# Optimization experiments

Hardware: AMD Instinct MI355X
Metric: run time of the kernel (lower is better)

## Reference

```python
import jax, jax.numpy as jnp
import numpy as np

N_NODES = 50000
N_EDGES = 800000
DIM = 128


def setup_inputs() -> dict:
    key = jax.random.key(0)
    k_x, k_e, k_w1, k_w2 = jax.random.split(key, 4)
    x = jax.random.normal(k_x, (N_NODES, DIM), dtype=jnp.float32)
    edge_index = jax.random.randint(k_e, (2, N_EDGES), 0, N_NODES, dtype=jnp.int64)
    scale = 1.0 / np.sqrt(DIM)
    W1 = jax.random.normal(k_w1, (DIM, DIM), dtype=jnp.float32) * scale
    b1 = jnp.zeros((DIM,), dtype=jnp.float32)
    W2 = jax.random.normal(k_w2, (DIM, DIM), dtype=jnp.float32) * scale
    b2 = jnp.zeros((DIM,), dtype=jnp.float32)
    return {"x": x, "edge_index": edge_index, "W1": W1, "b1": b1, "W2": W2, "b2": b2}


def _gcn_conv(x, W, b, src, dst, n_nodes):
    """PyG GCNConv: D^{-1/2}(A+I)D^{-1/2} (x @ W) + b, self-loops added."""
    h = x @ W  # [N, D]
    ones = jnp.ones(src.shape[0], dtype=h.dtype)
    # degree of A+I, counting incoming edges at target nodes plus self-loop
    deg = jax.ops.segment_sum(ones, dst, num_segments=n_nodes) + 1.0
    dinv = jax.lax.rsqrt(deg)  # [N]
    norm = dinv[src] * dinv[dst]  # [E]
    msgs = h[src] * norm[:, None]  # [E, D] gather (memory-bound)
    agg = jax.ops.segment_sum(msgs, dst, num_segments=n_nodes)  # scatter-add
    agg = agg + h * (dinv * dinv)[:, None]  # self-loop contribution
    return agg + b


def reference(x, edge_index, W1, b1, W2, b2):
    src, dst = edge_index[0], edge_index[1]
    n = x.shape[0]
    identity = x
    out = jax.nn.relu(_gcn_conv(x, W1, b1, src, dst, n))
    out = _gcn_conv(out, W2, b2, src, dst, n)
    return jax.nn.relu(out + identity)
```

## Files before the change

kernel.cpp:

```cpp
#include <hip/hip_runtime.h>

#define N_NODES 50000
#define N_EDGES 800000
#define DIM 128
#define NB 391
#define CAP 2560
#define NCH 7
#define BIN_CHUNK 4096
#define BIN_BLOCKS 196
#define GEMM_TILES 782

typedef unsigned int uint;
typedef unsigned short ushort;
typedef __attribute__((ext_vector_type(8))) __bf16 bf16x8;
typedef __attribute__((ext_vector_type(4))) float f32x4;

__device__ __forceinline__ uint f2bf(float f) {
    uint u = __float_as_uint(f);
    return (u + 0x7FFFu + ((u >> 16) & 1u)) >> 16;
}
__device__ __forceinline__ float2 bf2f2(uint u) {
    return make_float2(__uint_as_float(u << 16), __uint_as_float(u & 0xFFFF0000u));
}


__global__ __launch_bounds__(256) void prep_kernel(const float* __restrict__ W1,
                                                   const float* __restrict__ W2,
                                                   uint* __restrict__ Wt1,
                                                   uint* __restrict__ Wt2,
                                                   int* __restrict__ bincursor) {
    int idx = blockIdx.x * 256 + threadIdx.x;
    if (idx < 16384) {
        const float* W = (idx < 8192) ? W1 : W2;
        uint* Wt = (idx < 8192) ? Wt1 : Wt2;
        int i = idx & 8191;
        int n = i >> 6, k2 = i & 63;
        Wt[i] = f2bf(W[(2 * k2) * DIM + n]) | (f2bf(W[(2 * k2 + 1) * DIM + n]) << 16);
    } else {
        int b = idx - 16384;
        if (b < NB) bincursor[b] = b * CAP;
    }
}


template <bool ABF, bool SCALE, bool FROM_LDS>
__device__ __forceinline__ void gemm_tile(const void* Xv, const uint* __restrict__ sB,
                                          const uint* __restrict__ Wt,
                                          const float* __restrict__ dinv, int base,
                                          uint* __restrict__ Hout) {
    int t = threadIdx.x;
    int wv = t >> 6;
    int l = t & 63;
    int col = l & 15;
    int g = l >> 4;
    int lr = wv * 16 + col;
    int grow = base + lr;

    bf16x8 af[4];
    if (FROM_LDS) {
#pragma unroll
        for (int kk = 0; kk < 4; ++kk) {
            int ui = lr * 64 + ((kk * 16 + g * 4) ^ ((lr & 7) << 2));
            af[kk] = __builtin_bit_cast(bf16x8, *(const uint4*)&sB[ui]);
        }
    } else {
        int ar = grow > N_NODES - 1 ? N_NODES - 1 : grow;
        if (ABF) {
            const uint4* Xr = (const uint4*)((const uint*)Xv + (size_t)ar * 64);
#pragma unroll
            for (int kk = 0; kk < 4; ++kk) af[kk] = __builtin_bit_cast(bf16x8, Xr[kk * 4 + g]);
        } else {
            const float4* Xr = (const float4*)((const float*)Xv + (size_t)ar * DIM);
#pragma unroll
            for (int kk = 0; kk < 4; ++kk) {
                float4 x0 = Xr[kk * 8 + g * 2];
                float4 x1 = Xr[kk * 8 + g * 2 + 1];
                uint4 p;
                p.x = f2bf(x0.x) | (f2bf(x0.y) << 16);
                p.y = f2bf(x0.z) | (f2bf(x0.w) << 16);
                p.z = f2bf(x1.x) | (f2bf(x1.y) << 16);
                p.w = f2bf(x1.z) | (f2bf(x1.w) << 16);
                af[kk] = __builtin_bit_cast(bf16x8, p);
            }
        }
    }

    const uint4* Wr = (const uint4*)Wt;
    f32x4 acc[8];
#pragma unroll
    for (int n = 0; n < 8; ++n) acc[n] = (f32x4){0.f, 0.f, 0.f, 0.f};

#pragma unroll
    for (int n = 0; n < 8; ++n) {
        const uint4* wrow = Wr + (size_t)(n * 16 + col) * 16;
#pragma unroll
        for (int kk = 0; kk < 4; ++kk) {
            bf16x8 bf = __builtin_bit_cast(bf16x8, wrow[kk * 4 + g]);
            acc[n] = __builtin_amdgcn_mfma_f32_16x16x32_bf16(af[kk], bf, acc[n], 0, 0, 0);
        }
    }

#pragma unroll
    for (int j = 0; j < 4; ++j) {
        int row = base + wv * 16 + g * 4 + j;
        if (row < N_NODES) {
            float di = SCALE ? dinv[row] : 1.0f;
            ushort* hrow = (ushort*)(Hout + (size_t)row * 64);
#pragma unroll
            for (int n = 0; n < 8; ++n) {
                float v = SCALE ? acc[n][j] * di : acc[n][j];
                hrow[n * 16 + col] = (ushort)f2bf(v);
            }
        }
    }
}


__global__ __launch_bounds__(256) void bin_gemm1_kernel(const int* __restrict__ ei,
                                                        int* __restrict__ bincursor,
                                                        uint* __restrict__ pairs,
                                                        const float* __restrict__ x,
                                                        const uint* __restrict__ Wt1,
                                                        uint* __restrict__ Hs) {
    if (blockIdx.x >= BIN_BLOCKS) {
        int tile = blockIdx.x - BIN_BLOCKS;
        gemm_tile<false, false, false>((const void*)x, nullptr, Wt1, nullptr, tile * 64, Hs);
        return;
    }
    __shared__ int lh[NB];
    __shared__ int lbase[NB];
    int t = threadIdx.x;
    int eb = blockIdx.x * BIN_CHUNK;

    for (int b = t; b < NB; b += 256) lh[b] = 0;
    __syncthreads();

    int s_reg[16], d_reg[16];
#pragma unroll
    for (int i = 0; i < 16; ++i) {
        int e = eb + i * 256 + t;
        if (e < N_EDGES) {
            s_reg[i] = ei[e];
            d_reg[i] = ei[N_EDGES + e];
            atomicAdd(&lh[d_reg[i] >> 7], 1);
        } else {
            d_reg[i] = -1;
        }
    }
    __syncthreads();

    for (int b = t; b < NB; b += 256) {
        int c = lh[b];
        lbase[b] = c ? atomicAdd(&bincursor[b], c) : 0;
    }
    __syncthreads();
    for (int b = t; b < NB; b += 256) lh[b] = 0;
    __syncthreads();

#pragma unroll
    for (int i = 0; i < 16; ++i) {
        int d = d_reg[i];
        if (d >= 0) {
            int bin = d >> 7;
            int r = atomicAdd(&lh[bin], 1);
            pairs[lbase[bin] + r] = ((uint)s_reg[i] << 7) | (uint)(d & 127);
        }
    }
}


__global__ __launch_bounds__(256) void fill2_kernel(const uint* __restrict__ pairs,
                                                    const int* __restrict__ bincursor,
                                                    int* __restrict__ rowbeg,
                                                    int* __restrict__ rowend,
                                                    float* __restrict__ dinv,
                                                    int* __restrict__ csr_src) {
    __shared__ int cnt[128 * 8];
    __shared__ int nsum[128];
    __shared__ int nbase[128];
    int t = threadIdx.x;
    int blk = blockIdx.x;
    int bs = blk * CAP;
    int be = bincursor[blk];

    for (int i = t; i < 128 * 8; i += 256) cnt[i] = 0;
    __syncthreads();

    for (int p = bs + t; p < be; p += 256) {
        uint pr = pairs[p];
        atomicAdd(&cnt[(pr & 127u) * 8 + (pr >> 20)], 1);
    }
    __syncthreads();

    if (t < 128) {
        int s = 0;
#pragma unroll
        for (int c = 0; c < NCH; ++c) s += cnt[t * 8 + c];
        nsum[t] = s;
        nbase[t] = s;
    }
    __syncthreads();
#pragma unroll
    for (int off = 1; off < 128; off <<= 1) {
        int v = (t < 128 && t >= off) ? nbase[t - off] : 0;
        __syncthreads();
        if (t < 128) nbase[t] += v;
        __syncthreads();
    }

    if (t < 128) {
        int ex = nbase[t] - nsum[t];
        int node = blk * 128 + t;
        if (node < N_NODES) {
            rowbeg[node] = bs + ex;
            rowend[node] = bs + nbase[t];
            dinv[node] = rsqrtf((float)nsum[t] + 1.0f);
        }
        int run = ex;
#pragma unroll
        for (int c = 0; c < NCH; ++c) {
            int v = cnt[t * 8 + c];
            cnt[t * 8 + c] = run;
            run += v;
        }
    }
    __syncthreads();

    for (int p = bs + t; p < be; p += 256) {
        uint pr = pairs[p];
        int r = atomicAdd(&cnt[(pr & 127u) * 8 + (pr >> 20)], 1);
        csr_src[bs + r] = (int)(pr >> 7);
    }
}


template <bool DSRC>
__device__ __forceinline__ void agg_node(const int* __restrict__ rowbeg,
                                         const int* __restrict__ rowend,
                                         const int* __restrict__ csr_src,
                                         const uint* __restrict__ Hs,
                                         const float* __restrict__ dinv,
                                         const float* __restrict__ bias, int node, int li,
                                         float r[8]) {
    int beg = rowbeg[node];
    int end = rowend[node];
    float di = dinv[node];

    const uint4* H4 = (const uint4*)Hs;
    float a0, a1, a2, a3, a4, a5, a6, a7;
    {
        uint4 su = H4[(size_t)node * 16 + li];
        float2 v0 = bf2f2(su.x), v1 = bf2f2(su.y), v2 = bf2f2(su.z), v3 = bf2f2(su.w);
        float sf = DSRC ? di : 1.0f;
        a0 = sf * v0.x; a1 = sf * v0.y; a2 = sf * v1.x; a3 = sf * v1.y;
        a4 = sf * v2.x; a5 = sf * v2.y; a6 = sf * v3.x; a7 = sf * v3.y;
    }

#define ADDF8(u, f)                                                               \
    {                                                                             \
        float2 v0 = bf2f2(u.x), v1 = bf2f2(u.y), v2 = bf2f2(u.z), v3 = bf2f2(u.w);\
        a0 += f * v0.x; a1 += f * v0.y; a2 += f * v1.x; a3 += f * v1.y;           \
        a4 += f * v2.x; a5 += f * v2.y; a6 += f * v3.x; a7 += f * v3.y;           \
    }

    int e = beg;
    for (; e + 3 < end; e += 4) {
        int s0 = csr_src[e], s1 = csr_src[e + 1], s2 = csr_src[e + 2], s3 = csr_src[e + 3];
        uint4 u0 = H4[(size_t)s0 * 16 + li];
        uint4 u1 = H4[(size_t)s1 * 16 + li];
        uint4 u2 = H4[(size_t)s2 * 16 + li];
        uint4 u3 = H4[(size_t)s3 * 16 + li];
        float f0 = DSRC ? dinv[s0] : 1.0f;
        float f1 = DSRC ? dinv[s1] : 1.0f;
        float f2 = DSRC ? dinv[s2] : 1.0f;
        float f3 = DSRC ? dinv[s3] : 1.0f;
        ADDF8(u0, f0);
        ADDF8(u1, f1);
        ADDF8(u2, f2);
        ADDF8(u3, f3);
    }
    for (; e < end; ++e) {
        int s = csr_src[e];
        uint4 u = H4[(size_t)s * 16 + li];
        float f = DSRC ? dinv[s] : 1.0f;
        ADDF8(u, f);
    }
#undef ADDF8

    const float4* B4 = (const float4*)bias;
    float4 bb0 = B4[li * 2], bb1 = B4[li * 2 + 1];
    r[0] = a0 * di + bb0.x; r[1] = a1 * di + bb0.y;
    r[2] = a2 * di + bb0.z; r[3] = a3 * di + bb0.w;
    r[4] = a4 * di + bb1.x; r[5] = a5 * di + bb1.y;
    r[6] = a6 * di + bb1.z; r[7] = a7 * di + bb1.w;
}


__global__ __launch_bounds__(256) void aggemm_kernel(const int* __restrict__ rowbeg,
                                                     const int* __restrict__ rowend,
                                                     const int* __restrict__ csr_src,
                                                     const uint* __restrict__ Hs,
                                                     const float* __restrict__ dinv,
                                                     const float* __restrict__ b1,
                                                     const uint* __restrict__ Wt2,
                                                     uint* __restrict__ Hs2) {
    __shared__ uint sB[64 * 64];
    int t = threadIdx.x;
    int wv = t >> 6;
    int lane = t & 63;
    int grp = lane >> 4;
    int li = lane & 15;
    int base = blockIdx.x * 64;

#pragma unroll
    for (int p = 0; p < 4; ++p) {
        int row = p * 16 + wv * 4 + grp;
        int node = base + row;
        if (node < N_NODES) {
            float r[8];
            agg_node<true>(rowbeg, rowend, csr_src, Hs, dinv, b1, node, li, r);
            uint4 o;
            o.x = f2bf(fmaxf(r[0], 0.f)) | (f2bf(fmaxf(r[1], 0.f)) << 16);
            o.y = f2bf(fmaxf(r[2], 0.f)) | (f2bf(fmaxf(r[3], 0.f)) << 16);
            o.z = f2bf(fmaxf(r[4], 0.f)) | (f2bf(fmaxf(r[5], 0.f)) << 16);
            o.w = f2bf(fmaxf(r[6], 0.f)) | (f2bf(fmaxf(r[7], 0.f)) << 16);
            int ui = row * 64 + ((li * 4) ^ ((row & 7) << 2));
            *(uint4*)&sB[ui] = o;
        }
    }
    __syncthreads();

    gemm_tile<true, true, true>(nullptr, sB, Wt2, dinv, base, Hs2);
}


__global__ __launch_bounds__(256) void agg2_kernel(const int* __restrict__ rowbeg,
                                                   const int* __restrict__ rowend,
                                                   const int* __restrict__ csr_src,
                                                   const uint* __restrict__ Hs2,
                                                   const float* __restrict__ dinv,
                                                   const float* __restrict__ b2,
                                                   const float* __restrict__ resid,
                                                   float* __restrict__ out) {
    int wave = (int)((blockIdx.x * (size_t)blockDim.x + threadIdx.x) >> 6);
    int lane = threadIdx.x & 63;
    int grp = lane >> 4;
    int li = lane & 15;
    int node = wave * 4 + grp;

    float r[8];
    agg_node<false>(rowbeg, rowend, csr_src, Hs2, dinv, b2, node, li, r);

    const float4* R4 = (const float4*)(resid + (size_t)node * DIM);
    float4 x0 = R4[li * 2], x1 = R4[li * 2 + 1];
    r[0] += x0.x; r[1] += x0.y; r[2] += x0.z; r[3] += x0.w;
    r[4] += x1.x; r[5] += x1.y; r[6] += x1.z; r[7] += x1.w;

    float4* O4 = (float4*)(out + (size_t)node * DIM);
    O4[li * 2] = make_float4(fmaxf(r[0], 0.f), fmaxf(r[1], 0.f), fmaxf(r[2], 0.f),
                             fmaxf(r[3], 0.f));
    O4[li * 2 + 1] = make_float4(fmaxf(r[4], 0.f), fmaxf(r[5], 0.f), fmaxf(r[6], 0.f),
                                 fmaxf(r[7], 0.f));
}


extern "C" void kernel_launch(void* const* d_in, const int* in_sizes, int n_in,
                              void* d_out, int out_size, void* d_ws, size_t ws_size,
                              hipStream_t stream) {
    const float* x = (const float*)d_in[0];
    const int* edge_index = (const int*)d_in[1];
    const float* W1 = (const float*)d_in[2];
    const float* b1 = (const float*)d_in[3];
    const float* W2 = (const float*)d_in[4];
    const float* b2 = (const float*)d_in[5];
    float* out = (float*)d_out;

    char* ws = (char*)d_ws;
    int*   bincursor = (int*)(ws + 0);
    float* dinv      = (float*)(ws + (64 << 10));
    int*   rowbeg    = (int*)(ws + (320 << 10));
    int*   rowend    = (int*)(ws + (576 << 10));
    int*   csr_src   = (int*)(ws + (1 << 20));
    uint*  pairs     = (uint*)(ws + (6 << 20));
    uint*  Hs        = (uint*)(ws + (11 << 20));
    uint*  Hs2       = (uint*)(ws + (24 << 20));
    uint*  Wt1       = (uint*)(ws + (37 << 20));
    uint*  Wt2       = (uint*)(ws + (37 << 20) + (64 << 10));

    prep_kernel<<<66, 256, 0, stream>>>(W1, W2, Wt1, Wt2, bincursor);
    bin_gemm1_kernel<<<BIN_BLOCKS + GEMM_TILES, 256, 0, stream>>>(edge_index, bincursor, pairs,
                                                                  x, Wt1, Hs);
    fill2_kernel<<<NB, 256, 0, stream>>>(pairs, bincursor, rowbeg, rowend, dinv, csr_src);
    aggemm_kernel<<<GEMM_TILES, 256, 0, stream>>>(rowbeg, rowend, csr_src, Hs, dinv, b1, Wt2,
                                                  Hs2);
    agg2_kernel<<<3125, 256, 0, stream>>>(rowbeg, rowend, csr_src, Hs2, dinv, b2, x, out);
}
```

Measured before the change: 124.8 us.

## Halve aggregate-GEMM tile to 32 rows and unroll edge gather by 8

The fused layer-1 aggregation plus layer-2 GEMM kernel now processes 32 nodes per block instead of 64, doubling the grid. Its GEMM is split so each of the four waves computes a 16x64 quarter of the output. The edge-gather loop in agg_node is unrolled to 8 outstanding loads, with a 4-edge tail, to raise memory-level parallelism. The trade-off is more blocks with repeated W2 reads per block, and higher register pressure from the deeper unroll.

```diff
diff --git a/kernel.cpp b/kernel.cpp
--- a/kernel.cpp
+++ b/kernel.cpp
@@ -9,6 +9,7 @@
 #define BIN_CHUNK 4096
 #define BIN_BLOCKS 196
 #define GEMM_TILES 782
+#define AGG_TILES 1563
 
 typedef unsigned int uint;
 typedef unsigned short ushort;
@@ -43,46 +44,29 @@
 }
 
 
-template <bool ABF, bool SCALE, bool FROM_LDS>
-__device__ __forceinline__ void gemm_tile(const void* Xv, const uint* __restrict__ sB,
-                                          const uint* __restrict__ Wt,
-                                          const float* __restrict__ dinv, int base,
-                                          uint* __restrict__ Hout) {
+__device__ __forceinline__ void gemm_tile64(const float* __restrict__ X,
+                                            const uint* __restrict__ Wt, int base,
+                                            uint* __restrict__ Hout) {
     int t = threadIdx.x;
     int wv = t >> 6;
     int l = t & 63;
     int col = l & 15;
     int g = l >> 4;
-    int lr = wv * 16 + col;
-    int grow = base + lr;
+    int grow = base + wv * 16 + col;
+    int ar = grow > N_NODES - 1 ? N_NODES - 1 : grow;
 
     bf16x8 af[4];
-    if (FROM_LDS) {
-#pragma unroll
-        for (int kk = 0; kk < 4; ++kk) {
-            int ui = lr * 64 + ((kk * 16 + g * 4) ^ ((lr & 7) << 2));
-            af[kk] = __builtin_bit_cast(bf16x8, *(const uint4*)&sB[ui]);
-        }
-    } else {
-        int ar = grow > N_NODES - 1 ? N_NODES - 1 : grow;
-        if (ABF) {
-            const uint4* Xr = (const uint4*)((const uint*)Xv + (size_t)ar * 64);
-#pragma unroll
-            for (int kk = 0; kk < 4; ++kk) af[kk] = __builtin_bit_cast(bf16x8, Xr[kk * 4 + g]);
-        } else {
-            const float4* Xr = (const float4*)((const float*)Xv + (size_t)ar * DIM);
-#pragma unroll
-            for (int kk = 0; kk < 4; ++kk) {
-                float4 x0 = Xr[kk * 8 + g * 2];
-                float4 x1 = Xr[kk * 8 + g * 2 + 1];
-                uint4 p;
-                p.x = f2bf(x0.x) | (f2bf(x0.y) << 16);
-                p.y = f2bf(x0.z) | (f2bf(x0.w) << 16);
-                p.z = f2bf(x1.x) | (f2bf(x1.y) << 16);
-                p.w = f2bf(x1.z) | (f2bf(x1.w) << 16);
-                af[kk] = __builtin_bit_cast(bf16x8, p);
-            }
-        }
+    const float4* Xr = (const float4*)(X + (size_t)ar * DIM);
+#pragma unroll
+    for (int kk = 0; kk < 4; ++kk) {
+        float4 x0 = Xr[kk * 8 + g * 2];
+        float4 x1 = Xr[kk * 8 + g * 2 + 1];
+        uint4 p;
+        p.x = f2bf(x0.x) | (f2bf(x0.y) << 16);
+        p.y = f2bf(x0.z) | (f2bf(x0.w) << 16);
+        p.z = f2bf(x1.x) | (f2bf(x1.y) << 16);
+        p.w = f2bf(x1.z) | (f2bf(x1.w) << 16);
+        af[kk] = __builtin_bit_cast(bf16x8, p);
     }
 
     const uint4* Wr = (const uint4*)Wt;
@@ -104,12 +88,60 @@
     for (int j = 0; j < 4; ++j) {
         int row = base + wv * 16 + g * 4 + j;
         if (row < N_NODES) {
-            float di = SCALE ? dinv[row] : 1.0f;
             ushort* hrow = (ushort*)(Hout + (size_t)row * 64);
 #pragma unroll
-            for (int n = 0; n < 8; ++n) {
-                float v = SCALE ? acc[n][j] * di : acc[n][j];
-                hrow[n * 16 + col] = (ushort)f2bf(v);
+            for (int n = 0; n < 8; ++n) hrow[n * 16 + col] = (ushort)f2bf(acc[n][j]);
+        }
+    }
+}
+
+
+__device__ __forceinline__ void gemm_tile32_lds(const uint* __restrict__ sB,
+                                                const uint* __restrict__ Wt,
+                                                const float* __restrict__ dinv, int base,
+                                                uint* __restrict__ Hout) {
+    int t = threadIdx.x;
+    int wv = t >> 6;
+    int l = t & 63;
+    int col = l & 15;
+    int g = l >> 4;
+    int rh = wv & 1;
+    int ch = wv >> 1;
+    int lr = rh * 16 + col;
+
+    bf16x8 af[4];
+#pragma unroll
+    for (int kk = 0; kk < 4; ++kk) {
+        int ui = lr * 64 + ((kk * 16 + g * 4) ^ ((lr & 7) << 2));
+        af[kk] = __builtin_bit_cast(bf16x8, *(const uint4*)&sB[ui]);
+    }
+
+    const uint4* Wr = (const uint4*)Wt;
+    f32x4 acc[4];
+#pragma unroll
+    for (int nn = 0; nn < 4; ++nn) acc[nn] = (f32x4){0.f, 0.f, 0.f, 0.f};
+
+#pragma unroll
+    for (int nn = 0; nn < 4; ++nn) {
+        int n = ch * 4 + nn;
+        const uint4* wrow = Wr + (size_t)(n * 16 + col) * 16;
+#pragma unroll
+        for (int kk = 0; kk < 4; ++kk) {
+            bf16x8 bf = __builtin_bit_cast(bf16x8, wrow[kk * 4 + g]);
+            acc[nn] = __builtin_amdgcn_mfma_f32_16x16x32_bf16(af[kk], bf, acc[nn], 0, 0, 0);
+        }
+    }
+
+#pragma unroll
+    for (int j = 0; j < 4; ++j) {
+        int row = base + rh * 16 + g * 4 + j;
+        if (row < N_NODES) {
+            float di = dinv[row];
+            ushort* hrow = (ushort*)(Hout + (size_t)row * 64);
+#pragma unroll
+            for (int nn = 0; nn < 4; ++nn) {
+                int n = ch * 4 + nn;
+                hrow[n * 16 + col] = (ushort)f2bf(acc[nn][j] * di);
             }
         }
     }
@@ -123,8 +155,7 @@
                                                         const uint* __restrict__ Wt1,
                                                         uint* __restrict__ Hs) {
     if (blockIdx.x >= BIN_BLOCKS) {
-        int tile = blockIdx.x - BIN_BLOCKS;
-        gemm_tile<false, false, false>((const void*)x, nullptr, Wt1, nullptr, tile * 64, Hs);
+        gemm_tile64(x, Wt1, (blockIdx.x - BIN_BLOCKS) * 64, Hs);
         return;
     }
     __shared__ int lh[NB];
@@ -264,20 +295,32 @@
     }
 
     int e = beg;
-    for (; e + 3 < end; e += 4) {
-        int s0 = csr_src[e], s1 = csr_src[e + 1], s2 = csr_src[e + 2], s3 = csr_src[e + 3];
-        uint4 u0 = H4[(size_t)s0 * 16 + li];
-        uint4 u1 = H4[(size_t)s1 * 16 + li];
-        uint4 u2 = H4[(size_t)s2 * 16 + li];
-        uint4 u3 = H4[(size_t)s3 * 16 + li];
-        float f0 = DSRC ? dinv[s0] : 1.0f;
-        float f1 = DSRC ? dinv[s1] : 1.0f;
-        float f2 = DSRC ? dinv[s2] : 1.0f;
-        float f3 = DSRC ? dinv[s3] : 1.0f;
-        ADDF8(u0, f0);
-        ADDF8(u1, f1);
-        ADDF8(u2, f2);
-        ADDF8(u3, f3);
+    for (; e + 7 < end; e += 8) {
+        int s[8];
+#pragma unroll
+        for (int i = 0; i < 8; ++i) s[i] = csr_src[e + i];
+        uint4 u[8];
+#pragma unroll
+        for (int i = 0; i < 8; ++i) u[i] = H4[(size_t)s[i] * 16 + li];
+        float f[8];
+#pragma unroll
+        for (int i = 0; i < 8; ++i) f[i] = DSRC ? dinv[s[i]] : 1.0f;
+#pragma unroll
+        for (int i = 0; i < 8; ++i) ADDF8(u[i], f[i]);
+    }
+    if (e + 3 < end) {
+        int s[4];
+#pragma unroll
+        for (int i = 0; i < 4; ++i) s[i] = csr_src[e + i];
+        uint4 u[4];
+#pragma unroll
+        for (int i = 0; i < 4; ++i) u[i] = H4[(size_t)s[i] * 16 + li];
+        float f[4];
+#pragma unroll
+        for (int i = 0; i < 4; ++i) f[i] = DSRC ? dinv[s[i]] : 1.0f;
+#pragma unroll
+        for (int i = 0; i < 4; ++i) ADDF8(u[i], f[i]);
+        e += 4;
     }
     for (; e < end; ++e) {
         int s = csr_src[e];
@@ -304,16 +347,16 @@
                                                      const float* __restrict__ b1,
                                                      const uint* __restrict__ Wt2,
                                                      uint* __restrict__ Hs2) {
-    __shared__ uint sB[64 * 64];
+    __shared__ uint sB[32 * 64];
     int t = threadIdx.x;
     int wv = t >> 6;
     int lane = t & 63;
     int grp = lane >> 4;
     int li = lane & 15;
-    int base = blockIdx.x * 64;
-
-#pragma unroll
-    for (int p = 0; p < 4; ++p) {
+    int base = blockIdx.x * 32;
+
+#pragma unroll
+    for (int p = 0; p < 2; ++p) {
         int row = p * 16 + wv * 4 + grp;
         int node = base + row;
         if (node < N_NODES) {
@@ -330,7 +373,7 @@
     }
     __syncthreads();
 
-    gemm_tile<true, true, true>(nullptr, sB, Wt2, dinv, base, Hs2);
+    gemm_tile32_lds(sB, Wt2, dinv, base, Hs2);
 }
 
 
@@ -391,7 +434,7 @@
     bin_gemm1_kernel<<<BIN_BLOCKS + GEMM_TILES, 256, 0, stream>>>(edge_index, bincursor, pairs,
                                                                   x, Wt1, Hs);
     fill2_kernel<<<NB, 256, 0, stream>>>(pairs, bincursor, rowbeg, rowend, dinv, csr_src);
-    aggemm_kernel<<<GEMM_TILES, 256, 0, stream>>>(rowbeg, rowend, csr_src, Hs, dinv, b1, Wt2,
-                                                  Hs2);
+    aggemm_kernel<<<AGG_TILES, 256, 0, stream>>>(rowbeg, rowend, csr_src, Hs, dinv, b1, Wt2,
+                                                 Hs2);
     agg2_kernel<<<3125, 256, 0, stream>>>(rowbeg, rowend, csr_src, Hs2, dinv, b2, x, out);
 }
```

After: 123.6 us, median of 2. About the same (-0.9%).
